# Optimization experiments

Measured on AMD Instinct MI355X. Metric: run time of the kernel, lower is better.

## Reference

```python
import jax, jax.numpy as jnp
import numpy as np

EPS = 1e-6


def _rmsnorm(x, weight, eps=EPS):
    # float32 compute, cast back to input dtype, then scale (matches torch module)
    xf = x.astype(jnp.float32)
    rms = jax.lax.rsqrt(jnp.mean(xf * xf, axis=-1, keepdims=True) + eps)
    return (xf * rms).astype(x.dtype) * weight


def _block_attn_res(V, pseudo_query, norm_weight):
    # V: [n, b, t, d]; pseudo_query, norm_weight: [d]
    K = _rmsnorm(V, norm_weight)                          # [n,b,t,d]
    d = pseudo_query.shape[-1]
    logits = jnp.einsum('d,nbtd->nbt', pseudo_query, K) / jnp.sqrt(jnp.float32(d))
    attn = jax.nn.softmax(logits, axis=0)                 # softmax over block axis n
    return jnp.einsum('nbt,nbtd->btd', attn, V)           # [b,t,d]


def setup_inputs() -> dict:
    key = jax.random.key(0)
    ks = jax.random.split(key, 4)
    N, B, T, D = 7, 2, 4096, 2048
    return {
        'blocks': jax.random.normal(ks[0], (N, B, T, D), dtype=jnp.float32),
        'partial_block': jax.random.normal(ks[1], (B, T, D), dtype=jnp.float32),
        'pseudo_query_attn': jax.random.normal(ks[2], (D,), dtype=jnp.float32),
        'pseudo_query_mlp': jax.random.normal(ks[3], (D,), dtype=jnp.float32),
        'norm_weight_attn': jnp.ones((D,), dtype=jnp.float32),
        'norm_weight_mlp': jnp.ones((D,), dtype=jnp.float32),
    }


def reference(blocks, partial_block, pseudo_query_attn, pseudo_query_mlp,
              norm_weight_attn, norm_weight_mlp):
    # V = stack(blocks + [partial_block], dim=0): [N+1, B, T, D]
    V = jnp.concatenate([blocks, partial_block[None]], axis=0)
    h_attn = _block_attn_res(V, pseudo_query_attn, norm_weight_attn)
    h_mlp = _block_attn_res(V, pseudo_query_mlp, norm_weight_mlp)
    return (h_attn, h_mlp)
```

## Files before the change

### kernel.cpp

```cpp
#include <hip/hip_runtime.h>

#define NB 8
#define DDIM 2048
#define THREADS 512
#define NBLK 1024
#define NWAVES (THREADS / 64)

typedef float f32x4 __attribute__((ext_vector_type(4)));

__device__ __forceinline__ float wave_sum64(float x) {
    int t;
    t = __builtin_amdgcn_update_dpp(0, __float_as_int(x), 0x111, 0xf, 0xf, false);
    x += __int_as_float(t);
    t = __builtin_amdgcn_update_dpp(0, __float_as_int(x), 0x112, 0xf, 0xf, false);
    x += __int_as_float(t);
    t = __builtin_amdgcn_update_dpp(0, __float_as_int(x), 0x114, 0xf, 0xf, false);
    x += __int_as_float(t);
    t = __builtin_amdgcn_update_dpp(0, __float_as_int(x), 0x118, 0xf, 0xf, false);
    x += __int_as_float(t);
    t = __builtin_amdgcn_update_dpp(0, __float_as_int(x), 0x142, 0xa, 0xf, false);
    x += __int_as_float(t);
    t = __builtin_amdgcn_update_dpp(0, __float_as_int(x), 0x143, 0xc, 0xf, false);
    x += __int_as_float(t);
    return x;
}

__device__ __forceinline__ void barrier_lgkm() {
    asm volatile("s_waitcnt lgkmcnt(0)" ::: "memory");
    __builtin_amdgcn_s_barrier();
}

__global__ __launch_bounds__(THREADS, 4)
void block_attn_res_kernel(
    const float* __restrict__ blocks,
    const float* __restrict__ partial,
    const float* __restrict__ qa,
    const float* __restrict__ qm,
    const float* __restrict__ wa,
    const float* __restrict__ wm,
    float* __restrict__ out,
    int BT)
{
    const int tid = threadIdx.x;
    const int b   = blockIdx.x;
    const int c   = tid * 4;
    const size_t nStride = (size_t)BT * DDIM;
    const int rpb = BT / NBLK;

    __shared__ float red[NWAVES * 24];
    __shared__ float totl[24];

    const f32x4 qwa = *reinterpret_cast<const f32x4*>(qa + c) *
                      *reinterpret_cast<const f32x4*>(wa + c);
    const f32x4 qwm = *reinterpret_cast<const f32x4*>(qm + c) *
                      *reinterpret_cast<const f32x4*>(wm + c);

    f32x4 vA[NB], vB[NB];

    auto rowbase = [&](int i) -> size_t {
        return (size_t)(i * NBLK + b) * DDIM + c;
    };
    auto load_row = [&](f32x4* v, size_t rb) {
#pragma unroll
        for (int n = 0; n < NB; ++n) {
            const float* src = (n < NB - 1) ? (blocks + (size_t)n * nStride + rb)
                                            : (partial + rb);
            v[n] = *reinterpret_cast<const f32x4*>(src);
        }
    };

    const int wave = tid >> 6;
    const bool is63 = (tid & 63) == 63;

    auto process = [&](const f32x4* v, size_t rb) {
#pragma unroll
        for (int n = 0; n < NB; ++n) {
            float s = 0.f, pa = 0.f, pm = 0.f;
#pragma unroll
            for (int j = 0; j < 4; ++j) {
                s  += v[n][j] * v[n][j];
                pa += qwa[j]  * v[n][j];
                pm += qwm[j]  * v[n][j];
            }
            s  = wave_sum64(s);
            pa = wave_sum64(pa);
            pm = wave_sum64(pm);
            if (is63) {
                red[wave * 24 + n]      = s;
                red[wave * 24 + 8 + n]  = pa;
                red[wave * 24 + 16 + n] = pm;
            }
        }
        barrier_lgkm();
        if (tid < 24) {
            float s = 0.f;
#pragma unroll
            for (int w = 0; w < NWAVES; ++w) s += red[w * 24 + tid];
            totl[tid] = s;
        }
        barrier_lgkm();

        const float inv_sqrt_d = rsqrtf((float)DDIM);
        float lga[NB], lgm[NB];
#pragma unroll
        for (int n = 0; n < NB; ++n) {
            float rms = rsqrtf(totl[n] * (1.0f / DDIM) + 1e-6f);
            lga[n] = totl[8 + n]  * rms * inv_sqrt_d;
            lgm[n] = totl[16 + n] * rms * inv_sqrt_d;
        }
        float ma = lga[0], mm = lgm[0];
#pragma unroll
        for (int n = 1; n < NB; ++n) { ma = fmaxf(ma, lga[n]); mm = fmaxf(mm, lgm[n]); }

        f32x4 oa = (f32x4)(0.f), om = (f32x4)(0.f);
        float sa = 0.f, sm = 0.f;
#pragma unroll
        for (int n = 0; n < NB; ++n) {
            float ea = __expf(lga[n] - ma); sa += ea; oa += ea * v[n];
            float em = __expf(lgm[n] - mm); sm += em; om += em * v[n];
        }
        oa *= (1.f / sa);
        om *= (1.f / sm);
        *reinterpret_cast<f32x4*>(out + rb)           = oa;
        *reinterpret_cast<f32x4*>(out + nStride + rb) = om;
    };

    load_row(vA, rowbase(0));
#pragma unroll 1
    for (int i = 0; i < rpb; i += 2) {
        if (i + 1 < rpb) load_row(vB, rowbase(i + 1));
        process(vA, rowbase(i));
        if (i + 1 < rpb) {
            if (i + 2 < rpb) load_row(vA, rowbase(i + 2));
            process(vB, rowbase(i + 1));
        }
    }
}

extern "C" void kernel_launch(void* const* d_in, const int* in_sizes, int n_in,
                              void* d_out, int out_size, void* d_ws, size_t ws_size,
                              hipStream_t stream)
{
    const float* blocks  = (const float*)d_in[0];
    const float* partial = (const float*)d_in[1];
    const float* qa      = (const float*)d_in[2];
    const float* qm      = (const float*)d_in[3];
    const float* wa      = (const float*)d_in[4];
    const float* wm      = (const float*)d_in[5];
    float* out = (float*)d_out;

    const int D  = in_sizes[2];
    const int BT = in_sizes[1] / D;

    dim3 grid(NBLK), block(THREADS);
    hipLaunchKernelGGL(block_attn_res_kernel, grid, block, 0, stream,
                       blocks, partial, qa, qm, wa, wm, out, BT);
}
```

Measured before the change: 140.2 us.

## Restructure to 256-thread blocks with double-buffered single-barrier reductions

Halves the threads per block so each thread covers two 4-float slices of a row. The grid now has BT/4 blocks that each handle exactly four rows in a fully unrolled, software-pipelined sequence. The cross-wave reduction uses alternating shared buffers, and every thread sums the per-wave partials itself, which removes the second barrier per row. This trims synchronisation and serial reduction on a kernel that is essentially bandwidth-bound, at the cost of more live registers and a lower occupancy bound.

New measurement: 138.4 us. Within noise of the previous version (-1.3%).

```diff
diff --git a/kernel.cpp b/kernel.cpp
--- a/kernel.cpp
+++ b/kernel.cpp
@@ -2,8 +2,8 @@
 
 #define NB 8
 #define DDIM 2048
-#define THREADS 512
-#define NBLK 1024
+#define THREADS 256
+#define NROWS 4
 #define NWAVES (THREADS / 64)
 
 typedef float f32x4 __attribute__((ext_vector_type(4)));
@@ -30,7 +30,7 @@
     __builtin_amdgcn_s_barrier();
 }
 
-__global__ __launch_bounds__(THREADS, 4)
+__global__ __launch_bounds__(THREADS, 2)
 void block_attn_res_kernel(
     const float* __restrict__ blocks,
     const float* __restrict__ partial,
@@ -43,98 +43,111 @@
 {
     const int tid = threadIdx.x;
     const int b   = blockIdx.x;
-    const int c   = tid * 4;
+    const int nblk = gridDim.x;
+    const int c0 = tid * 4;
+    const int c1 = c0 + DDIM / 2;
     const size_t nStride = (size_t)BT * DDIM;
-    const int rpb = BT / NBLK;
 
-    __shared__ float red[NWAVES * 24];
-    __shared__ float totl[24];
+    __shared__ float red[2][NWAVES * 24];
+    __shared__ float totl[2][24];
 
-    const f32x4 qwa = *reinterpret_cast<const f32x4*>(qa + c) *
-                      *reinterpret_cast<const f32x4*>(wa + c);
-    const f32x4 qwm = *reinterpret_cast<const f32x4*>(qm + c) *
-                      *reinterpret_cast<const f32x4*>(wm + c);
+    const f32x4 qwa0 = *reinterpret_cast<const f32x4*>(qa + c0) *
+                       *reinterpret_cast<const f32x4*>(wa + c0);
+    const f32x4 qwa1 = *reinterpret_cast<const f32x4*>(qa + c1) *
+                       *reinterpret_cast<const f32x4*>(wa + c1);
+    const f32x4 qwm0 = *reinterpret_cast<const f32x4*>(qm + c0) *
+                       *reinterpret_cast<const f32x4*>(wm + c0);
+    const f32x4 qwm1 = *reinterpret_cast<const f32x4*>(qm + c1) *
+                       *reinterpret_cast<const f32x4*>(wm + c1);
 
-    f32x4 vA[NB], vB[NB];
+    f32x4 vA[NB][2], vB[NB][2];
 
-    auto rowbase = [&](int i) -> size_t {
-        return (size_t)(i * NBLK + b) * DDIM + c;
+    auto rowbase = [&](int g) -> size_t {
+        return (size_t)(g * nblk + b) * DDIM;
     };
-    auto load_row = [&](f32x4* v, size_t rb) {
+    auto load_row = [&](f32x4 (*v)[2], size_t rb) {
 #pragma unroll
         for (int n = 0; n < NB; ++n) {
             const float* src = (n < NB - 1) ? (blocks + (size_t)n * nStride + rb)
                                             : (partial + rb);
-            v[n] = *reinterpret_cast<const f32x4*>(src);
+            v[n][0] = *reinterpret_cast<const f32x4*>(src + c0);
+            v[n][1] = *reinterpret_cast<const f32x4*>(src + c1);
         }
     };
 
     const int wave = tid >> 6;
     const bool is63 = (tid & 63) == 63;
 
-    auto process = [&](const f32x4* v, size_t rb) {
+    auto process = [&](const f32x4 (*v)[2], float* redb, float* totb, size_t rb) {
 #pragma unroll
         for (int n = 0; n < NB; ++n) {
             float s = 0.f, pa = 0.f, pm = 0.f;
 #pragma unroll
             for (int j = 0; j < 4; ++j) {
-                s  += v[n][j] * v[n][j];
-                pa += qwa[j]  * v[n][j];
-                pm += qwm[j]  * v[n][j];
+                s  += v[n][0][j] * v[n][0][j] + v[n][1][j] * v[n][1][j];
+                pa += qwa0[j] * v[n][0][j] + qwa1[j] * v[n][1][j];
+                pm += qwm0[j] * v[n][0][j] + qwm1[j] * v[n][1][j];
             }
             s  = wave_sum64(s);
             pa = wave_sum64(pa);
             pm = wave_sum64(pm);
             if (is63) {
-                red[wave * 24 + n]      = s;
-                red[wave * 24 + 8 + n]  = pa;
-                red[wave * 24 + 16 + n] = pm;
+                redb[wave * 24 + n]      = s;
+                redb[wave * 24 + 8 + n]  = pa;
+                redb[wave * 24 + 16 + n] = pm;
             }
         }
         barrier_lgkm();
-        if (tid < 24) {
-            float s = 0.f;
+
+        float t24[24];
+        {
+            const f32x4* r4 = reinterpret_cast<const f32x4*>(redb);
 #pragma unroll
-            for (int w = 0; w < NWAVES; ++w) s += red[w * 24 + tid];
-            totl[tid] = s;
+            for (int g = 0; g < 6; ++g) {
+                f32x4 x = r4[g] + r4[6 + g] + r4[12 + g] + r4[18 + g];
+                t24[4 * g + 0] = x.x; t24[4 * g + 1] = x.y;
+                t24[4 * g + 2] = x.z; t24[4 * g + 3] = x.w;
+            }
         }
-        barrier_lgkm();
+        (void)totb;
 
         const float inv_sqrt_d = rsqrtf((float)DDIM);
         float lga[NB], lgm[NB];
 #pragma unroll
         for (int n = 0; n < NB; ++n) {
-            float rms = rsqrtf(totl[n] * (1.0f / DDIM) + 1e-6f);
-            lga[n] = totl[8 + n]  * rms * inv_sqrt_d;
-            lgm[n] = totl[16 + n] * rms * inv_sqrt_d;
+            float rms = rsqrtf(t24[n] * (1.0f / DDIM) + 1e-6f);
+            lga[n] = t24[8 + n]  * rms * inv_sqrt_d;
+            lgm[n] = t24[16 + n] * rms * inv_sqrt_d;
         }
         float ma = lga[0], mm = lgm[0];
 #pragma unroll
         for (int n = 1; n < NB; ++n) { ma = fmaxf(ma, lga[n]); mm = fmaxf(mm, lgm[n]); }
 
-        f32x4 oa = (f32x4)(0.f), om = (f32x4)(0.f);
+        f32x4 oa0 = (f32x4)(0.f), oa1 = (f32x4)(0.f);
+        f32x4 om0 = (f32x4)(0.f), om1 = (f32x4)(0.f);
         float sa = 0.f, sm = 0.f;
 #pragma unroll
         for (int n = 0; n < NB; ++n) {
-            float ea = __expf(lga[n] - ma); sa += ea; oa += ea * v[n];
-            float em = __expf(lgm[n] - mm); sm += em; om += em * v[n];
+            float ea = __expf(lga[n] - ma); sa += ea;
+            float em = __expf(lgm[n] - mm); sm += em;
+            oa0 += ea * v[n][0]; oa1 += ea * v[n][1];
+            om0 += em * v[n][0]; om1 += em * v[n][1];
         }
-        oa *= (1.f / sa);
-        om *= (1.f / sm);
-        *reinterpret_cast<f32x4*>(out + rb)           = oa;
-        *reinterpret_cast<f32x4*>(out + nStride + rb) = om;
+        const float ra = 1.f / sa, rm = 1.f / sm;
+        *reinterpret_cast<f32x4*>(out + rb + c0)            = oa0 * ra;
+        *reinterpret_cast<f32x4*>(out + rb + c1)            = oa1 * ra;
+        *reinterpret_cast<f32x4*>(out + nStride + rb + c0)  = om0 * rm;
+        *reinterpret_cast<f32x4*>(out + nStride + rb + c1)  = om1 * rm;
     };
 
     load_row(vA, rowbase(0));
-#pragma unroll 1
-    for (int i = 0; i < rpb; i += 2) {
-        if (i + 1 < rpb) load_row(vB, rowbase(i + 1));
-        process(vA, rowbase(i));
-        if (i + 1 < rpb) {
-            if (i + 2 < rpb) load_row(vA, rowbase(i + 2));
-            process(vB, rowbase(i + 1));
-        }
-    }
+    load_row(vB, rowbase(1));
+    process(vA, red[0], totl[0], rowbase(0));
+    load_row(vA, rowbase(2));
+    process(vB, red[1], totl[1], rowbase(1));
+    load_row(vB, rowbase(3));
+    process(vA, red[0], totl[0], rowbase(2));
+    process(vB, red[1], totl[1], rowbase(3));
 }
 
 extern "C" void kernel_launch(void* const* d_in, const int* in_sizes, int n_in,
@@ -152,7 +165,7 @@
     const int D  = in_sizes[2];
     const int BT = in_sizes[1] / D;
 
-    dim3 grid(NBLK), block(THREADS);
+    dim3 grid(BT / NROWS), block(THREADS);
     hipLaunchKernelGGL(block_attn_res_kernel, grid, block, 0, stream,
                        blocks, partial, qa, qm, wa, wm, out, BT);
 }
```

## Launch one workgroup per row instead of persistent double-buffered loop

Applied to the files above, without the earlier changes.

Replaces the persistent grid of 1024 workgroups, each looping over several rows with register double-buffering, with one workgroup per (b,t) row. All threads now do the final cross-wave reduction redundantly with vectorized LDS reads, which removes the second barrier. Outputs are written with nontemporal stores and the occupancy hint is raised to 6. This relies on hardware occupancy to hide memory latency instead of explicit prefetch, at the cost of more workgroup launches and more per-workgroup setup.

New measurement: 124.1 us. 1.13x faster.

```diff
diff --git a/kernel.cpp b/kernel.cpp
--- a/kernel.cpp
+++ b/kernel.cpp
@@ -3,7 +3,6 @@
 #define NB 8
 #define DDIM 2048
 #define THREADS 512
-#define NBLK 1024
 #define NWAVES (THREADS / 64)
 
 typedef float f32x4 __attribute__((ext_vector_type(4)));
@@ -25,12 +24,7 @@
     return x;
 }
 
-__device__ __forceinline__ void barrier_lgkm() {
-    asm volatile("s_waitcnt lgkmcnt(0)" ::: "memory");
-    __builtin_amdgcn_s_barrier();
-}
-
-__global__ __launch_bounds__(THREADS, 4)
+__global__ __launch_bounds__(THREADS, 6)
 void block_attn_res_kernel(
     const float* __restrict__ blocks,
     const float* __restrict__ partial,
@@ -41,100 +35,88 @@
     float* __restrict__ out,
     int BT)
 {
+    const int row = blockIdx.x;
     const int tid = threadIdx.x;
-    const int b   = blockIdx.x;
     const int c   = tid * 4;
+
+    const size_t rowBase = (size_t)row * DDIM;
     const size_t nStride = (size_t)BT * DDIM;
-    const int rpb = BT / NBLK;
 
     __shared__ float red[NWAVES * 24];
-    __shared__ float totl[24];
+
+    f32x4 v[NB];
+    {
+        const float* base = blocks + rowBase + c;
+#pragma unroll
+        for (int n = 0; n < NB - 1; ++n)
+            v[n] = *reinterpret_cast<const f32x4*>(base + (size_t)n * nStride);
+        v[NB - 1] = *reinterpret_cast<const f32x4*>(partial + rowBase + c);
+    }
 
     const f32x4 qwa = *reinterpret_cast<const f32x4*>(qa + c) *
                       *reinterpret_cast<const f32x4*>(wa + c);
     const f32x4 qwm = *reinterpret_cast<const f32x4*>(qm + c) *
                       *reinterpret_cast<const f32x4*>(wm + c);
 
-    f32x4 vA[NB], vB[NB];
-
-    auto rowbase = [&](int i) -> size_t {
-        return (size_t)(i * NBLK + b) * DDIM + c;
-    };
-    auto load_row = [&](f32x4* v, size_t rb) {
-#pragma unroll
-        for (int n = 0; n < NB; ++n) {
-            const float* src = (n < NB - 1) ? (blocks + (size_t)n * nStride + rb)
-                                            : (partial + rb);
-            v[n] = *reinterpret_cast<const f32x4*>(src);
-        }
-    };
-
     const int wave = tid >> 6;
     const bool is63 = (tid & 63) == 63;
-
-    auto process = [&](const f32x4* v, size_t rb) {
 #pragma unroll
-        for (int n = 0; n < NB; ++n) {
-            float s = 0.f, pa = 0.f, pm = 0.f;
+    for (int n = 0; n < NB; ++n) {
+        float s = 0.f, pa = 0.f, pm = 0.f;
 #pragma unroll
-            for (int j = 0; j < 4; ++j) {
-                s  += v[n][j] * v[n][j];
-                pa += qwa[j]  * v[n][j];
-                pm += qwm[j]  * v[n][j];
-            }
-            s  = wave_sum64(s);
-            pa = wave_sum64(pa);
-            pm = wave_sum64(pm);
-            if (is63) {
-                red[wave * 24 + n]      = s;
-                red[wave * 24 + 8 + n]  = pa;
-                red[wave * 24 + 16 + n] = pm;
-            }
+        for (int j = 0; j < 4; ++j) {
+            s  += v[n][j] * v[n][j];
+            pa += qwa[j]  * v[n][j];
+            pm += qwm[j]  * v[n][j];
         }
-        barrier_lgkm();
-        if (tid < 24) {
-            float s = 0.f;
-#pragma unroll
-            for (int w = 0; w < NWAVES; ++w) s += red[w * 24 + tid];
-            totl[tid] = s;
-        }
-        barrier_lgkm();
-
-        const float inv_sqrt_d = rsqrtf((float)DDIM);
-        float lga[NB], lgm[NB];
-#pragma unroll
-        for (int n = 0; n < NB; ++n) {
-            float rms = rsqrtf(totl[n] * (1.0f / DDIM) + 1e-6f);
-            lga[n] = totl[8 + n]  * rms * inv_sqrt_d;
-            lgm[n] = totl[16 + n] * rms * inv_sqrt_d;
-        }
-        float ma = lga[0], mm = lgm[0];
-#pragma unroll
-        for (int n = 1; n < NB; ++n) { ma = fmaxf(ma, lga[n]); mm = fmaxf(mm, lgm[n]); }
-
-        f32x4 oa = (f32x4)(0.f), om = (f32x4)(0.f);
-        float sa = 0.f, sm = 0.f;
-#pragma unroll
-        for (int n = 0; n < NB; ++n) {
-            float ea = __expf(lga[n] - ma); sa += ea; oa += ea * v[n];
-            float em = __expf(lgm[n] - mm); sm += em; om += em * v[n];
-        }
-        oa *= (1.f / sa);
-        om *= (1.f / sm);
-        *reinterpret_cast<f32x4*>(out + rb)           = oa;
-        *reinterpret_cast<f32x4*>(out + nStride + rb) = om;
-    };
-
-    load_row(vA, rowbase(0));
-#pragma unroll 1
-    for (int i = 0; i < rpb; i += 2) {
-        if (i + 1 < rpb) load_row(vB, rowbase(i + 1));
-        process(vA, rowbase(i));
-        if (i + 1 < rpb) {
-            if (i + 2 < rpb) load_row(vA, rowbase(i + 2));
-            process(vB, rowbase(i + 1));
+        s  = wave_sum64(s);
+        pa = wave_sum64(pa);
+        pm = wave_sum64(pm);
+        if (is63) {
+            red[wave * 24 + n]      = s;
+            red[wave * 24 + 8 + n]  = pa;
+            red[wave * 24 + 16 + n] = pm;
         }
     }
+    __syncthreads();
+
+    float t24[24];
+    {
+        const f32x4* r4 = reinterpret_cast<const f32x4*>(red);
+#pragma unroll
+        for (int g = 0; g < 6; ++g) {
+            f32x4 x = r4[g];
+#pragma unroll
+            for (int w = 1; w < NWAVES; ++w) x += r4[w * 6 + g];
+            t24[4 * g + 0] = x.x; t24[4 * g + 1] = x.y;
+            t24[4 * g + 2] = x.z; t24[4 * g + 3] = x.w;
+        }
+    }
+
+    const float inv_sqrt_d = rsqrtf((float)DDIM);
+    float lga[NB], lgm[NB];
+#pragma unroll
+    for (int n = 0; n < NB; ++n) {
+        float rms = rsqrtf(t24[n] * (1.0f / DDIM) + 1e-6f);
+        lga[n] = t24[8 + n]  * rms * inv_sqrt_d;
+        lgm[n] = t24[16 + n] * rms * inv_sqrt_d;
+    }
+    float ma = lga[0], mm = lgm[0];
+#pragma unroll
+    for (int n = 1; n < NB; ++n) { ma = fmaxf(ma, lga[n]); mm = fmaxf(mm, lgm[n]); }
+
+    f32x4 oa = (f32x4)(0.f), om = (f32x4)(0.f);
+    float sa = 0.f, sm = 0.f;
+#pragma unroll
+    for (int n = 0; n < NB; ++n) {
+        float ea = __expf(lga[n] - ma); sa += ea; oa += ea * v[n];
+        float em = __expf(lgm[n] - mm); sm += em; om += em * v[n];
+    }
+    oa *= (1.f / sa);
+    om *= (1.f / sm);
+
+    __builtin_nontemporal_store(oa, reinterpret_cast<f32x4*>(out + rowBase + c));
+    __builtin_nontemporal_store(om, reinterpret_cast<f32x4*>(out + nStride + rowBase + c));
 }
 
 extern "C" void kernel_launch(void* const* d_in, const int* in_sizes, int n_in,
@@ -152,7 +134,7 @@
     const int D  = in_sizes[2];
     const int BT = in_sizes[1] / D;
 
-    dim3 grid(NBLK), block(THREADS);
+    dim3 grid(BT), block(THREADS);
     hipLaunchKernelGGL(block_attn_res_kernel, grid, block, 0, stream,
                        blocks, partial, qa, qm, wa, wm, out, BT);
 }
```
